# Kernel optimization log

Hardware: AMD Instinct MI355X
Metric: run time of the kernel (lower is better)

The kernel has to match this reference:

```python
import jax, jax.numpy as jnp
import numpy as np

B = 8192
IN = 2048
H = 2048


def setup_inputs() -> dict:
    key = jax.random.key(0)
    ks = jax.random.split(key, 7)
    s_in = 1.0 / np.sqrt(IN)
    s_h = 1.0 / np.sqrt(H)
    inp = jax.random.normal(ks[0], (B, IN), jnp.float32)
    h0 = jax.random.normal(ks[1], (B, H), jnp.float32)
    c0 = jax.random.normal(ks[2], (B, H), jnp.float32)
    # Packed gate weights: columns ordered [i, f, o, g], each block size H.
    # Equivalent to the 8 separate nn.Linear layers (i_w,f_w,o_w,g_w / i_u,f_u,o_u,g_u).
    W = jax.random.uniform(ks[3], (IN, 4 * H), jnp.float32, -s_in, s_in)
    b_w = jax.random.uniform(ks[4], (4 * H,), jnp.float32, -s_in, s_in)
    U = jax.random.uniform(ks[5], (H, 4 * H), jnp.float32, -s_h, s_h)
    b_u = jax.random.uniform(ks[6], (4 * H,), jnp.float32, -s_h, s_h)
    return {"inp": inp, "h0": h0, "c0": c0, "W": W, "b_w": b_w, "U": U, "b_u": b_u}


def reference(inp, h0, c0, W, b_w, U, b_u):
    # Two big GEMMs instead of eight small ones; identical math.
    gates = inp @ W + b_w + h0 @ U + b_u  # [B, 4H]
    i_g, f_g, o_g, g_g = jnp.split(gates, 4, axis=-1)
    i = jax.nn.sigmoid(i_g)
    f = jax.nn.sigmoid(f_g)
    o = jax.nn.sigmoid(o_g)
    g = jnp.tanh(g_g)
    c = f * c0 + i * g
    h = o * jnp.tanh(c)
    return (h, c)
```

## Files before the change

kernel.cpp:

```cpp
#include <hip/hip_runtime.h>
#include <hip/hip_bf16.h>

#define B_DIM 8192
#define IN_DIM 2048
#define H_DIM 2048
#define K_DIM 4096
#define N4H   8192
#define NT    64

using short8 = __attribute__((ext_vector_type(8))) short;
using f32x4  = __attribute__((ext_vector_type(4))) float;
using u16x4  = __attribute__((ext_vector_type(4))) unsigned short;

__device__ __forceinline__ unsigned short f2bf(float f) {
  union { float f; unsigned int u; } v; v.f = f;
  unsigned int u = v.u;
  return (unsigned short)((u + 0x7FFFu + ((u >> 16) & 1u)) >> 16);
}

__global__ __launch_bounds__(256) void pack_a(const float* __restrict__ inp,
                                              const float* __restrict__ h0,
                                              unsigned short* __restrict__ Ap) {
  size_t idx = ((size_t)blockIdx.x * 256 + threadIdx.x) * 4;
  int b = (int)(idx >> 12);
  int k = (int)(idx & 4095);
  const float* src = (k < IN_DIM) ? (inp + (size_t)b * IN_DIM + k)
                                  : (h0  + (size_t)b * H_DIM + (k - IN_DIM));
  float4 v = *(const float4*)src;
  u16x4 o = { f2bf(v.x), f2bf(v.y), f2bf(v.z), f2bf(v.w) };
  *(u16x4*)&Ap[idx] = o;
}

__global__ __launch_bounds__(256) void pack_b(const float* __restrict__ W,
                                              const float* __restrict__ U,
                                              unsigned short* __restrict__ Bp) {
  __shared__ float tile[64][17];
  const int c0 = blockIdx.x * 16;
  const int k0 = blockIdx.y * 64;
  const int gate  = (c0 >> 4) & 3;
  const int jbase = (c0 >> 6) * 16;
  const int colbase = gate * 2048 + jbase;
  const int t  = threadIdx.x;
  const int cc = t & 15;
  const int r0 = t >> 4;
#pragma unroll
  for (int rr = 0; rr < 4; ++rr) {
    int k = k0 + r0 + rr * 16;
    const float* src = (k < IN_DIM) ? (W + (size_t)k * N4H)
                                    : (U + (size_t)(k - IN_DIM) * N4H);
    tile[r0 + rr * 16][cc] = src[colbase + cc];
  }
  __syncthreads();
  const int c   = t >> 4;
  const int kk0 = (t & 15) * 4;
  u16x4 o = { f2bf(tile[kk0 + 0][c]), f2bf(tile[kk0 + 1][c]),
              f2bf(tile[kk0 + 2][c]), f2bf(tile[kk0 + 3][c]) };
  *(u16x4*)&Bp[(size_t)(c0 + c) * K_DIM + k0 + kk0] = o;
}

__global__ __launch_bounds__(512, 2) void lstm_gemm(
    const unsigned short* __restrict__ Ap,
    const unsigned short* __restrict__ Bp,
    const float* __restrict__ c0,
    const float* __restrict__ b_w,
    const float* __restrict__ b_u,
    float* __restrict__ out) {
  __shared__ unsigned short lds[65536];

  const int t     = threadIdx.x;
  const int lane  = t & 63;
  const int wid   = t >> 6;
  const int wr    = wid >> 2;
  const int wc    = wid & 3;
  const int laneM = lane & 15;
  const int laneG = lane >> 4;

  const int wg  = blockIdx.x;
  const int swz = (wg & 7) * 128 + (wg >> 3);
  const int bm  = swz >> 5;
  const int bn  = swz & 31;

  const int rt   = t >> 3;
  const int gt   = t & 7;
  const int gsw  = gt ^ (rt & 7);
  const unsigned short* gA = Ap + (size_t)(bm * 256 + rt) * K_DIM + gsw * 8;
  const unsigned short* gB = Bp + (size_t)(bn * 256 + rt) * K_DIM + gsw * 8;

#define STAGE(gptr, ldsoff)                                                   \
  __builtin_amdgcn_global_load_lds(                                           \
      (const __attribute__((address_space(1))) void*)(gptr),                  \
      (__attribute__((address_space(3))) void*)&lds[(ldsoff) + t * 8], 16, 0, 0)

#define VMCNT(n) asm volatile("s_waitcnt vmcnt(" #n ")" ::: "memory")
#define BARF()                                                                \
  do {                                                                        \
    asm volatile("" ::: "memory");                                            \
    __builtin_amdgcn_s_barrier();                                             \
    asm volatile("" ::: "memory");                                            \
  } while (0)

  const int sbit = laneM & 7;
  int aoff[2], boff[2];
#pragma unroll
  for (int kk = 0; kk < 2; ++kk) {
    aoff[kk] = wr * 8192 + laneM * 64 + ((kk * 4 + laneG) ^ sbit) * 8;
    boff[kk] = 16384 + (wc >> 1) * 8192 + ((wc & 1) * 64 + laneM) * 64
               + ((kk * 4 + laneG) ^ sbit) * 8;
  }

#define RD_AF(AF, BASE, PH)                                                   \
  _Pragma("unroll")                                                           \
  for (int i = 0; i < 2; ++i)                                                 \
    _Pragma("unroll")                                                         \
    for (int kk = 0; kk < 2; ++kk)                                            \
      AF[i][kk] = *(const short8*)&lds[(BASE) + aoff[kk] + (2 * (PH) + i) * 1024];

#define RD_BF(BASE)                                                           \
  _Pragma("unroll")                                                           \
  for (int n = 0; n < 4; ++n)                                                 \
    _Pragma("unroll")                                                         \
    for (int kk = 0; kk < 2; ++kk)                                            \
      bfr[n][kk] = *(const short8*)&lds[(BASE) + boff[kk] + n * 1024];

#define MFMA16(Q, AF)                                                         \
  __builtin_amdgcn_s_setprio(1);                                              \
  _Pragma("unroll")                                                           \
  for (int i = 0; i < 2; ++i)                                                 \
    _Pragma("unroll")                                                         \
    for (int n = 0; n < 4; ++n)                                               \
      _Pragma("unroll")                                                       \
      for (int kk = 0; kk < 2; ++kk)                                          \
        acc[2 * (Q) + i][n] = __builtin_amdgcn_mfma_f32_16x16x32_bf16(        \
            AF[i][kk], bfr[n][kk], acc[2 * (Q) + i][n], 0, 0, 0);             \
  __builtin_amdgcn_s_setprio(0)

  f32x4 acc[8][4];
#pragma unroll
  for (int m = 0; m < 8; ++m)
#pragma unroll
    for (int n = 0; n < 4; ++n)
      acc[m][n] = (f32x4){0.f, 0.f, 0.f, 0.f};

  short8 af0[2][2], af1[2][2], bfr[4][2];

  const int j = (bn * 4 + wc) * 16 + laneM;
  float bias[4];
#pragma unroll
  for (int g = 0; g < 4; ++g)
    bias[g] = b_w[g * 2048 + j] + b_u[g * 2048 + j];
  asm volatile("s_waitcnt vmcnt(0)" ::: "memory");

  STAGE(gA,               0);
  STAGE(gA + 128 * K_DIM, 8192);
  STAGE(gB,               16384);
  STAGE(gB +  64 * K_DIM, 16384 + 4096);
  STAGE(gB + 128 * K_DIM, 16384 + 8192);
  STAGE(gB + 192 * K_DIM, 16384 + 12288);
  STAGE(gA +  64 * K_DIM, 4096);
  STAGE(gA + 192 * K_DIM, 12288);
  VMCNT(2);
  BARF();
  RD_AF(af0, 0, 0);
  RD_BF(0);

#pragma unroll 1
  for (int kt = 0; kt < NT - 1; ++kt) {
    const int cb = (kt & 1) << 15;
    const int db = cb ^ 32768;
    const unsigned short* gA1 = gA + (kt + 1) * 64;
    const unsigned short* gB1 = gB + (kt + 1) * 64;
    STAGE(gA1,               db + 0);
    STAGE(gA1 + 128 * K_DIM, db + 8192);
    BARF();
    RD_AF(af1, cb, 1);
    MFMA16(0, af0);
    STAGE(gB1,               db + 16384);
    STAGE(gB1 +  64 * K_DIM, db + 16384 + 4096);
    STAGE(gB1 + 128 * K_DIM, db + 16384 + 8192);
    STAGE(gB1 + 192 * K_DIM, db + 16384 + 12288);
    VMCNT(6);
    BARF();
    RD_AF(af0, cb, 2);
    MFMA16(1, af1);
    STAGE(gA1 +  64 * K_DIM, db + 4096);
    STAGE(gA1 + 192 * K_DIM, db + 12288);
    BARF();
    RD_AF(af1, cb, 3);
    MFMA16(2, af0);
    VMCNT(2);
    BARF();
    RD_AF(af0, db, 0);
    MFMA16(3, af1);
    RD_BF(db);
  }

  {
    RD_AF(af1, 32768, 1);
    MFMA16(0, af0);
    VMCNT(0);
    BARF();
    RD_AF(af0, 32768, 2);
    MFMA16(1, af1);
    RD_AF(af1, 32768, 3);
    MFMA16(2, af0);
    MFMA16(3, af1);
  }

  const int rbase = bm * 256 + wr * 128 + laneG * 4;
  float* outH = out;
  float* outC = out + (size_t)B_DIM * H_DIM;
#pragma unroll
  for (int m = 0; m < 8; ++m) {
#pragma unroll
    for (int r = 0; r < 4; ++r) {
      const int bi = rbase + m * 16 + r;
      const size_t off = (size_t)bi * H_DIM + j;
      float ig = acc[m][0][r] + bias[0];
      float fg = acc[m][1][r] + bias[1];
      float og = acc[m][2][r] + bias[2];
      float gg = acc[m][3][r] + bias[3];
      float iv = 1.f / (1.f + __expf(-ig));
      float fv = 1.f / (1.f + __expf(-fg));
      float ov = 1.f / (1.f + __expf(-og));
      float gv = 2.f / (1.f + __expf(-2.f * gg)) - 1.f;
      float cv = fv * c0[off] + iv * gv;
      float tc = 2.f / (1.f + __expf(-2.f * cv)) - 1.f;
      outH[off] = ov * tc;
      outC[off] = cv;
    }
  }
}

extern "C" void kernel_launch(void* const* d_in, const int* in_sizes, int n_in,
                              void* d_out, int out_size, void* d_ws, size_t ws_size,
                              hipStream_t stream) {
  const float* inp = (const float*)d_in[0];
  const float* h0  = (const float*)d_in[1];
  const float* c0  = (const float*)d_in[2];
  const float* W   = (const float*)d_in[3];
  const float* b_w = (const float*)d_in[4];
  const float* U   = (const float*)d_in[5];
  const float* b_u = (const float*)d_in[6];
  float* out = (float*)d_out;

  unsigned short* Ap = (unsigned short*)d_ws;
  unsigned short* Bp = Ap + (size_t)B_DIM * K_DIM;

  pack_a<<<(B_DIM * K_DIM / 4) / 256, 256, 0, stream>>>(inp, h0, Ap);
  dim3 gb(N4H / 16, K_DIM / 64);
  pack_b<<<gb, 256, 0, stream>>>(W, U, Bp);
  lstm_gemm<<<1024, 512, 0, stream>>>(Ap, Bp, c0, b_w, b_u, out);
}
```

Before: 565.5 us.

## Drop A-fragment double-buffering in registers and serialize LDS reads with MFMA

Replaces the two alternating register buffers for A fragments with a single buffer. Each phase now reads from LDS and then runs its MFMAs, with extra barriers between them, instead of prefetching the next fragment while the current MFMAs execute. This lowers register pressure, but it removes the overlap between LDS reads and matrix math and adds barriers, so LDS latency is more exposed. The epilogue and the first-tile handling change to match.

```diff
diff --git a/kernel.cpp b/kernel.cpp
--- a/kernel.cpp
+++ b/kernel.cpp
@@ -108,12 +108,12 @@
                + ((kk * 4 + laneG) ^ sbit) * 8;
   }
 
-#define RD_AF(AF, BASE, PH)                                                   \
+#define RD_AF(BASE, PH)                                                       \
   _Pragma("unroll")                                                           \
   for (int i = 0; i < 2; ++i)                                                 \
     _Pragma("unroll")                                                         \
     for (int kk = 0; kk < 2; ++kk)                                            \
-      AF[i][kk] = *(const short8*)&lds[(BASE) + aoff[kk] + (2 * (PH) + i) * 1024];
+      af[i][kk] = *(const short8*)&lds[(BASE) + aoff[kk] + (2 * (PH) + i) * 1024];
 
 #define RD_BF(BASE)                                                           \
   _Pragma("unroll")                                                           \
@@ -122,7 +122,7 @@
     for (int kk = 0; kk < 2; ++kk)                                            \
       bfr[n][kk] = *(const short8*)&lds[(BASE) + boff[kk] + n * 1024];
 
-#define MFMA16(Q, AF)                                                         \
+#define MFMA16(Q)                                                             \
   __builtin_amdgcn_s_setprio(1);                                              \
   _Pragma("unroll")                                                           \
   for (int i = 0; i < 2; ++i)                                                 \
@@ -131,7 +131,7 @@
       _Pragma("unroll")                                                       \
       for (int kk = 0; kk < 2; ++kk)                                          \
         acc[2 * (Q) + i][n] = __builtin_amdgcn_mfma_f32_16x16x32_bf16(        \
-            AF[i][kk], bfr[n][kk], acc[2 * (Q) + i][n], 0, 0, 0);             \
+            af[i][kk], bfr[n][kk], acc[2 * (Q) + i][n], 0, 0, 0);             \
   __builtin_amdgcn_s_setprio(0)
 
   f32x4 acc[8][4];
@@ -141,7 +141,7 @@
     for (int n = 0; n < 4; ++n)
       acc[m][n] = (f32x4){0.f, 0.f, 0.f, 0.f};
 
-  short8 af0[2][2], af1[2][2], bfr[4][2];
+  short8 af[2][2], bfr[4][2];
 
   const int j = (bn * 4 + wc) * 16 + laneM;
   float bias[4];
@@ -160,8 +160,6 @@
   STAGE(gA + 192 * K_DIM, 12288);
   VMCNT(2);
   BARF();
-  RD_AF(af0, 0, 0);
-  RD_BF(0);
 
 #pragma unroll 1
   for (int kt = 0; kt < NT - 1; ++kt) {
@@ -169,41 +167,47 @@
     const int db = cb ^ 32768;
     const unsigned short* gA1 = gA + (kt + 1) * 64;
     const unsigned short* gB1 = gB + (kt + 1) * 64;
+    RD_BF(cb);
+    RD_AF(cb, 0);
     STAGE(gA1,               db + 0);
     STAGE(gA1 + 128 * K_DIM, db + 8192);
     BARF();
-    RD_AF(af1, cb, 1);
-    MFMA16(0, af0);
+    MFMA16(0);
+    BARF();
+    RD_AF(cb, 1);
     STAGE(gB1,               db + 16384);
     STAGE(gB1 +  64 * K_DIM, db + 16384 + 4096);
     STAGE(gB1 + 128 * K_DIM, db + 16384 + 8192);
     STAGE(gB1 + 192 * K_DIM, db + 16384 + 12288);
     VMCNT(6);
     BARF();
-    RD_AF(af0, cb, 2);
-    MFMA16(1, af1);
+    MFMA16(1);
+    BARF();
+    RD_AF(cb, 2);
     STAGE(gA1 +  64 * K_DIM, db + 4096);
     STAGE(gA1 + 192 * K_DIM, db + 12288);
     BARF();
-    RD_AF(af1, cb, 3);
-    MFMA16(2, af0);
+    MFMA16(2);
+    BARF();
+    RD_AF(cb, 3);
     VMCNT(2);
     BARF();
-    RD_AF(af0, db, 0);
-    MFMA16(3, af1);
-    RD_BF(db);
+    MFMA16(3);
+    BARF();
   }
 
   {
-    RD_AF(af1, 32768, 1);
-    MFMA16(0, af0);
+    RD_BF(32768);
+    RD_AF(32768, 0);
+    MFMA16(0);
+    RD_AF(32768, 1);
+    MFMA16(1);
     VMCNT(0);
     BARF();
-    RD_AF(af0, 32768, 2);
-    MFMA16(1, af1);
-    RD_AF(af1, 32768, 3);
-    MFMA16(2, af0);
-    MFMA16(3, af1);
+    RD_AF(32768, 2);
+    MFMA16(2);
+    RD_AF(32768, 3);
+    MFMA16(3);
   }
 
   const int rbase = bm * 256 + wr * 128 + laneG * 4;
```

New measurement: 592.3 us. 1.05x slower.
